# Optimization experiments

Hardware: AMD Instinct MI355X
Metric: run time of the kernel (lower is better)

The kernel has to match this reference:

```python
import jax, jax.numpy as jnp
import numpy as np

N = 2048
D = 512
E = 65536
THR = 0.0          # config['edge_threshold']
CLUSTER_RANGE = 2
NEG_SLOPE = 0.01   # F.leaky_relu default


def segment_softmax(x, seg, num_segments):
    # torch_geometric.utils.softmax over segments (here: source nodes)
    m = jax.ops.segment_max(x, seg, num_segments)
    e = jnp.exp(x - m[seg])
    s = jax.ops.segment_sum(e, seg, num_segments)
    return e / (s[seg] + 1e-16)


def setup_inputs() -> dict:
    key = jax.random.key(0)
    k1, k2, k3 = jax.random.split(key, 3)
    embedding = jax.random.normal(k1, (N, D), dtype=jnp.float32)
    edge_index = jax.random.randint(k2, (2, E), 0, N)
    src, dst = edge_index[0], edge_index[1]
    edge_matrix = jnp.zeros((N, N), jnp.float32).at[src, dst].set(1.0)
    edge_matrix_weight = edge_matrix  # unit edge weights
    W_score = (jax.random.normal(k3, (2 * D, 1), dtype=jnp.float32) / np.sqrt(2.0 * D)).astype(jnp.float32)
    b_score = jnp.zeros((1,), jnp.float32)
    return {"embedding": embedding, "edge_index": edge_index,
            "edge_matrix": edge_matrix, "edge_matrix_weight": edge_matrix_weight,
            "W_score": W_score, "b_score": b_score}


def reference(embedding, edge_index, edge_matrix, edge_matrix_weight, W_score, b_score):
    n = embedding.shape[0]
    dt = embedding.dtype
    diag = jnp.eye(n, dtype=bool)

    # connectivity fitness: Z @ Z.T with L2-normalized rows
    Z = embedding / jnp.maximum(jnp.linalg.norm(embedding, axis=-1, keepdims=True), 1e-12)
    connectivity_M = Z @ Z.T                                   # [N,N]

    # structural fitness: edge-score -> leaky_relu -> segment softmax -> dense scatter
    src, dst = edge_index[0], edge_index[1]
    x_pair = jnp.concatenate([embedding[src], embedding[dst]], axis=-1) @ W_score + b_score  # [E,1]
    x_score = jax.nn.leaky_relu(x_pair[:, 0], NEG_SLOPE)
    x_score = segment_softmax(x_score, src, n)
    structure_M = jnp.zeros((n, n), dt).at[src, dst].add(x_score)
    fitness = connectivity_M + structure_M                     # fitness_mode == 'both_j'

    # Generate_clusters (cluster_range = 2)
    mat = jnp.where(diag, 0.0, edge_matrix)
    mat = jnp.where(fitness < THR, 0.0, mat)
    A1 = mat
    A2 = (jnp.where(diag, 0.0, A1 @ A1) > 0.5).astype(dt)
    A2 = jnp.maximum(A2 - A1, 0.0)
    cluster_matrix = ((A1 + A2) > 0).astype(dt)

    # Cluster_assignment: mean fitness per cluster matrix, nan -> 0
    scores = jnp.zeros((n,), dt)
    for A in (A1, A2):
        deg = A.sum(-1)
        scores = scores + jnp.where(deg > 0, (fitness * A).sum(-1) / jnp.where(deg > 0, deg, 1.0), 0.0)
    cluster_scores = scores / CLUSTER_RANGE

    # Select_clusters (overlap=True, pick_all=True): local extrema over A1 neighborhood
    local_extrema = (cluster_scores[:, None] - A1 * cluster_scores[None, :]) > 0
    is_cluster = local_extrema.all(axis=-1)                    # boolean cluster-center mask

    # Generate_assignment_matrix (mask-based instead of column slicing; removed
    # 'reduced' columns are kept as zero columns so shapes stay static)
    S = cluster_matrix
    S_f = cluster_matrix * fitness
    reduced = (S * is_cluster.astype(dt)[None, :]).sum(-1) > 0   # member of a selected cluster
    isolated = S.sum(0) == 0
    reduced = reduced | isolated
    keeping = (~is_cluster) & (~reduced)

    S = jnp.where(keeping[None, :], 0.0, S)
    S_f = jnp.where(keeping[None, :], 0.0, S_f)
    S = jnp.where(diag, 1.0, S)
    S_f = jnp.where(diag, 1.0, S_f)
    col_keep = (~reduced).astype(dt)[None, :]
    S = S * col_keep
    S_f = S_f * col_keep

    # pooling_mode == 'mean': pooled embedding = S_w.T @ X
    pooled = S_f.T @ embedding                                  # [N, D], zero rows = removed nodes
    return pooled
```

## Files before the change

### kernel.cpp

```cpp
#include <hip/hip_runtime.h>
#include <cstdint>
#include <cstddef>

typedef unsigned long long u64;
typedef unsigned int u32;
typedef _Float16 half8 __attribute__((ext_vector_type(8)));
typedef float f32x4 __attribute__((ext_vector_type(4)));

#define NN 2048
#define DD 512
#define EE 65536
#define NW 32

__device__ __forceinline__ u32 fmap(float x) {
    u32 u = __float_as_uint(x);
    return (u & 0x80000000u) ? ~u : (u | 0x80000000u);
}
__device__ __forceinline__ float funmap(u32 u) {
    return (u & 0x80000000u) ? __uint_as_float(u ^ 0x80000000u) : __uint_as_float(~u);
}

__global__ __launch_bounds__(256) void k_node(const float* __restrict__ emb,
                                              const float* __restrict__ Wsc,
                                              float* inv_norm, float* av, float* cv,
                                              _Float16* __restrict__ zh,
                                              _Float16* __restrict__ zl,
                                              u32* mmax, float* ssum,
                                              u64* centerBits, u64* colAny, u64* EBw) {
    int n = blockIdx.x;
    int t = threadIdx.x;
    if (n < 256) EBw[n * 256 + t] = 0ull;
    else if (n < 264) { int idx = (n - 256) * 256 + t; mmax[idx] = 0u; ssum[idx] = 0.0f; }
    else if (n == 264 && t < NW) { centerBits[t] = 0ull; colAny[t] = 0ull; }

    const float* row = emb + (size_t)n * DD;
    float ss = 0.f, aa = 0.f, cc = 0.f;
    for (int d = t; d < DD; d += 256) {
        float v = row[d];
        ss += v * v;
        aa += v * Wsc[d];
        cc += v * Wsc[DD + d];
    }
    for (int off = 32; off; off >>= 1) {
        ss += __shfl_down(ss, off);
        aa += __shfl_down(aa, off);
        cc += __shfl_down(cc, off);
    }
    __shared__ float red[3][4];
    __shared__ float s_inv;
    int wid = t >> 6, lane = t & 63;
    if (lane == 0) { red[0][wid] = ss; red[1][wid] = aa; red[2][wid] = cc; }
    __syncthreads();
    if (t == 0) {
        float s = 0.f, a = 0.f, c = 0.f;
        for (int w = 0; w < 4; w++) { s += red[0][w]; a += red[1][w]; c += red[2][w]; }
        float iv = 1.0f / fmaxf(sqrtf(s), 1e-12f);
        inv_norm[n] = iv;
        s_inv = iv;
        av[n] = a;
        cv[n] = c;
    }
    __syncthreads();
    float iv = s_inv;
    for (int d = t; d < DD; d += 256) {
        float z = row[d] * iv;
        _Float16 h = (_Float16)z;
        _Float16 l = (_Float16)(z - (float)h);
        zh[(size_t)n * DD + d] = h;
        zl[(size_t)n * DD + d] = l;
    }
}

__device__ __forceinline__ float edge_score(const int* ei, const float* av, const float* cv,
                                            float b0, int e, int* src, int* dst) {
    int s = ei[e], d = ei[EE + e];
    *src = s; *dst = d;
    float x = av[s] + cv[d] + b0;
    return x > 0.f ? x : 0.01f * x;
}

__global__ __launch_bounds__(256) void k_edgeA(const int* __restrict__ ei,
                                               const float* __restrict__ av,
                                               const float* __restrict__ cv,
                                               const float* __restrict__ bsc,
                                               u32* mmax, u64* EBw) {
    int e = blockIdx.x * 256 + threadIdx.x;
    if (e >= EE) return;
    int s, d;
    float x = edge_score(ei, av, cv, bsc[0], e, &s, &d);
    atomicMax(&mmax[s], fmap(x));
    atomicOr(&EBw[(size_t)s * NW + (d >> 6)], 1ull << (d & 63));
}

__global__ __launch_bounds__(256) void k_edge_sum(const int* __restrict__ ei,
                                                  const float* __restrict__ av,
                                                  const float* __restrict__ cv,
                                                  const float* __restrict__ bsc,
                                                  const u32* __restrict__ mmax, float* ssum) {
    int e = blockIdx.x * 256 + threadIdx.x;
    if (e >= EE) return;
    int s, d;
    float x = edge_score(ei, av, cv, bsc[0], e, &s, &d);
    float w = expf(x - funmap(mmax[s]));
    atomicAdd(&ssum[s], w);
}

__global__ __launch_bounds__(256) void k_edge_scatter(const int* __restrict__ ei,
                                                      const float* __restrict__ av,
                                                      const float* __restrict__ cv,
                                                      const float* __restrict__ bsc,
                                                      const u32* __restrict__ mmax,
                                                      const float* __restrict__ ssum,
                                                      float* fit) {
    int e = blockIdx.x * 256 + threadIdx.x;
    if (e >= EE) return;
    int s, d;
    float x = edge_score(ei, av, cv, bsc[0], e, &s, &d);
    float w = expf(x - funmap(mmax[s])) / (ssum[s] + 1e-16f);
    atomicAdd(&fit[(size_t)s * NN + d], w);
}

#define BK 64
__global__ __launch_bounds__(512) void k_fitness(const _Float16* __restrict__ zh,
                                                 const _Float16* __restrict__ zl,
                                                 float* __restrict__ fit) {
    __shared__ _Float16 Ah[128 * BK];
    __shared__ _Float16 Al[128 * BK];
    __shared__ _Float16 Bh[128 * BK];
    __shared__ _Float16 Bl[128 * BK];
    int tid = threadIdx.x;
    int wid = tid >> 6, lane = tid & 63;
    int wr = wid >> 2, wc = wid & 3;
    int I = blockIdx.y * 128, J = blockIdx.x * 128;
    int lr = lane & 15;
    int q = lane >> 4;
    f32x4 acc[4][2] = {};

    int rl0 = tid >> 3, sl0 = tid & 7;
    int rl1 = (512 + tid) >> 3, sl1 = tid & 7;
    int ks0 = ((sl0 ^ (rl0 & 7)) << 3);
    int ks1 = ((sl1 ^ (rl1 & 7)) << 3);
    size_t gA0 = (size_t)(I + rl0) * DD + ks0, gB0 = (size_t)(J + rl0) * DD + ks0;
    size_t gA1 = (size_t)(I + rl1) * DD + ks1, gB1 = (size_t)(J + rl1) * DD + ks1;
    int lo0 = rl0 * BK + sl0 * 8, lo1 = rl1 * BK + sl1 * 8;

    {
        half8 a0 = *reinterpret_cast<const half8*>(&zh[gA0]);
        half8 a1 = *reinterpret_cast<const half8*>(&zh[gA1]);
        half8 l0 = *reinterpret_cast<const half8*>(&zl[gA0]);
        half8 l1 = *reinterpret_cast<const half8*>(&zl[gA1]);
        half8 b0 = *reinterpret_cast<const half8*>(&zh[gB0]);
        half8 b1 = *reinterpret_cast<const half8*>(&zh[gB1]);
        half8 m0 = *reinterpret_cast<const half8*>(&zl[gB0]);
        half8 m1 = *reinterpret_cast<const half8*>(&zl[gB1]);
        *reinterpret_cast<half8*>(&Ah[lo0]) = a0;
        *reinterpret_cast<half8*>(&Ah[lo1]) = a1;
        *reinterpret_cast<half8*>(&Al[lo0]) = l0;
        *reinterpret_cast<half8*>(&Al[lo1]) = l1;
        *reinterpret_cast<half8*>(&Bh[lo0]) = b0;
        *reinterpret_cast<half8*>(&Bh[lo1]) = b1;
        *reinterpret_cast<half8*>(&Bl[lo0]) = m0;
        *reinterpret_cast<half8*>(&Bl[lo1]) = m1;
    }
    __syncthreads();

    for (int k0 = 0; k0 < DD; k0 += BK) {
        half8 nA0, nA1, nAl0, nAl1, nB0, nB1, nBl0, nBl1;
        bool hasNext = (k0 + BK) < DD;
        if (hasNext) {
            int kn = k0 + BK;
            nA0  = *reinterpret_cast<const half8*>(&zh[gA0 + kn]);
            nA1  = *reinterpret_cast<const half8*>(&zh[gA1 + kn]);
            nAl0 = *reinterpret_cast<const half8*>(&zl[gA0 + kn]);
            nAl1 = *reinterpret_cast<const half8*>(&zl[gA1 + kn]);
            nB0  = *reinterpret_cast<const half8*>(&zh[gB0 + kn]);
            nB1  = *reinterpret_cast<const half8*>(&zh[gB1 + kn]);
            nBl0 = *reinterpret_cast<const half8*>(&zl[gB0 + kn]);
            nBl1 = *reinterpret_cast<const half8*>(&zl[gB1 + kn]);
        }
#pragma unroll
        for (int kk = 0; kk < 2; kk++) {
            half8 a_h[4], a_l[4], b_h[2], b_l[2];
#pragma unroll
            for (int f = 0; f < 4; f++) {
                int ra = wr * 64 + f * 16 + lr;
                int ca = (kk * 4 + q) ^ (ra & 7);
                int oa = ra * BK + ca * 8;
                a_h[f] = *reinterpret_cast<const half8*>(&Ah[oa]);
                a_l[f] = *reinterpret_cast<const half8*>(&Al[oa]);
            }
#pragma unroll
            for (int v = 0; v < 2; v++) {
                int rb = wc * 32 + v * 16 + lr;
                int cb = (kk * 4 + q) ^ (rb & 7);
                int ob = rb * BK + cb * 8;
                b_h[v] = *reinterpret_cast<const half8*>(&Bh[ob]);
                b_l[v] = *reinterpret_cast<const half8*>(&Bl[ob]);
            }
#pragma unroll
            for (int u = 0; u < 4; u++)
#pragma unroll
                for (int v = 0; v < 2; v++) {
                    acc[u][v] = __builtin_amdgcn_mfma_f32_16x16x32_f16(a_h[u], b_h[v], acc[u][v], 0, 0, 0);
                    acc[u][v] = __builtin_amdgcn_mfma_f32_16x16x32_f16(a_h[u], b_l[v], acc[u][v], 0, 0, 0);
                    acc[u][v] = __builtin_amdgcn_mfma_f32_16x16x32_f16(a_l[u], b_h[v], acc[u][v], 0, 0, 0);
                }
        }
        if (hasNext) {
            __syncthreads();
            *reinterpret_cast<half8*>(&Ah[lo0]) = nA0;
            *reinterpret_cast<half8*>(&Ah[lo1]) = nA1;
            *reinterpret_cast<half8*>(&Al[lo0]) = nAl0;
            *reinterpret_cast<half8*>(&Al[lo1]) = nAl1;
            *reinterpret_cast<half8*>(&Bh[lo0]) = nB0;
            *reinterpret_cast<half8*>(&Bh[lo1]) = nB1;
            *reinterpret_cast<half8*>(&Bl[lo0]) = nBl0;
            *reinterpret_cast<half8*>(&Bl[lo1]) = nBl1;
            __syncthreads();
        }
    }
#pragma unroll
    for (int u = 0; u < 4; u++) {
        int r = I + wr * 64 + u * 16 + q * 4;
#pragma unroll
        for (int v = 0; v < 2; v++) {
            int c = J + wc * 32 + v * 16 + lr;
#pragma unroll
            for (int i2 = 0; i2 < 4; i2++)
                fit[(size_t)(r + i2) * NN + c] = acc[u][v][i2];
        }
    }
}

__global__ void k_bits(const u64* __restrict__ EBw, const float* __restrict__ fit,
                       u64* __restrict__ A1w) {
    int i = blockIdx.x;
    int t = threadIdx.x;
    int lane = t & 63, wv = t >> 6;
    for (int q = 0; q < 8; q++) {
        int j = q * 256 + t;
        u64 eb = EBw[(size_t)i * NW + (j >> 6)];
        float f = fit[(size_t)i * NN + j];
        bool pred = ((eb >> (j & 63)) & 1) && (j != i) && (f >= 0.f);
        u64 word = __ballot(pred);
        if (lane == 0) A1w[i * NW + q * 4 + wv] = word;
    }
}

__global__ __launch_bounds__(256) void k_paths2s(const u64* __restrict__ A1w,
                                                 const float* __restrict__ fit,
                                                 u64* __restrict__ A2w, u64* __restrict__ CLw,
                                                 float* cs) {
    int i = blockIdx.x;
    __shared__ u64 rowA[NW];
    __shared__ u64 rowA2[NW];
    __shared__ u64 part[8][NW];
    int t = threadIdx.x;
    if (t < NW) rowA[t] = A1w[i * NW + t];
    __syncthreads();
    int g = t >> 5, w = t & 31;
    u64 acc = 0;
    for (int ww = 0; ww < 4; ww++) {
        u64 bits = rowA[g * 4 + ww];
        int kbase = (g * 4 + ww) * 64;
        while (bits) {
            int k = __ffsll((unsigned long long)bits) - 1;
            bits &= bits - 1;
            acc |= A1w[(size_t)(kbase + k) * NW + w];
        }
    }
    part[g][w] = acc;
    __syncthreads();
    if (g == 0) {
        u64 p2 = part[0][w];
#pragma unroll
        for (int gg = 1; gg < 8; gg++) p2 |= part[gg][w];
        if ((i >> 6) == w) p2 &= ~(1ull << (i & 63));
        u64 a1 = rowA[w];
        u64 a2 = p2 & ~a1;
        u64 cl = a1 | a2;
        A2w[i * NW + w] = a2;
        CLw[i * NW + w] = cl;
        rowA2[w] = a2;
    }
    __syncthreads();
    float s1 = 0.f, s2 = 0.f;
    int d1 = 0, d2 = 0;
    for (int q = 0; q < 8; q++) {
        int j = q * 256 + t;
        float f = fit[(size_t)i * NN + j];
        int ww = j >> 6, b = j & 63;
        u64 a1 = rowA[ww], a2 = rowA2[ww];
        if ((a1 >> b) & 1) { s1 += f; d1++; }
        if ((a2 >> b) & 1) { s2 += f; d2++; }
    }
    for (int off = 32; off; off >>= 1) {
        s1 += __shfl_down(s1, off);
        s2 += __shfl_down(s2, off);
        d1 += __shfl_down(d1, off);
        d2 += __shfl_down(d2, off);
    }
    __shared__ float rs1[4], rs2[4];
    __shared__ int rd1[4], rd2[4];
    int wid = t >> 6, lane = t & 63;
    if (lane == 0) { rs1[wid] = s1; rs2[wid] = s2; rd1[wid] = d1; rd2[wid] = d2; }
    __syncthreads();
    if (t == 0) {
        float S1 = 0.f, S2 = 0.f; int D1 = 0, D2 = 0;
        for (int w2 = 0; w2 < 4; w2++) { S1 += rs1[w2]; S2 += rs2[w2]; D1 += rd1[w2]; D2 += rd2[w2]; }
        float v1 = D1 > 0 ? S1 / (float)D1 : 0.f;
        float v2 = D2 > 0 ? S2 / (float)D2 : 0.f;
        cs[i] = 0.5f * (v1 + v2);
    }
}

__global__ __launch_bounds__(256) void k_extcol(const u64* __restrict__ A1w,
                                                const u64* __restrict__ CLw,
                                                const float* __restrict__ cs,
                                                unsigned char* is_c, u64* centerBits,
                                                u64* colAny) {
    int i = blockIdx.x, t = threadIdx.x;
    __shared__ u64 part[8][NW];
    if (i < 64) {
        int sub = t >> 5, w = t & 31;
        u64 acc = 0;
#pragma unroll
        for (int k = 0; k < 4; k++) {
            int r = i * 32 + sub + k * 8;
            acc |= CLw[(size_t)r * NW + w];
        }
        part[sub][w] = acc;
    }
    float ci = cs[i];
    int ok = 1;
    for (int q = 0; q < 8; q++) {
        int j = q * 256 + t;
        u64 a1 = A1w[i * NW + (j >> 6)];
        float other = ((a1 >> (j & 63)) & 1) ? cs[j] : 0.0f;
        ok &= ((ci - other) > 0.0f) ? 1 : 0;
    }
    int all = __syncthreads_and(ok);
    if (t == 0) {
        is_c[i] = (unsigned char)(all ? 1 : 0);
        if (all) atomicOr(&centerBits[i >> 6], 1ull << (i & 63));
    }
    if (i < 64 && t < NW) {
        u64 v = part[0][t];
#pragma unroll
        for (int s = 1; s < 8; s++) v |= part[s][t];
        atomicOr(&colAny[t], v);
    }
}

__global__ __launch_bounds__(256) void k_pooled(const float* __restrict__ fit,
                                                const float* __restrict__ emb,
                                                const u64* __restrict__ CLw,
                                                const u64* __restrict__ centerBits,
                                                const u64* __restrict__ colAny,
                                                const unsigned char* __restrict__ is_c,
                                                float* __restrict__ out) {
    int j = blockIdx.x;
    int t = threadIdx.x;
    bool red = ((colAny[j >> 6] >> (j & 63)) & 1ull) == 0ull;
    for (int w = 0; w < NW; w++) red |= (CLw[(size_t)j * NW + w] & centerBits[w]) != 0ull;
    const float2* embj = reinterpret_cast<const float2*>(emb + (size_t)j * DD);
    float2* outj = reinterpret_cast<float2*>(out + (size_t)j * DD);
    bool active = is_c[j] && !red;
    if (!active) {
        float dg = red ? 0.0f : 1.0f;
        float2 v = embj[t];
        float2 o; o.x = v.x * dg; o.y = v.y * dg;
        outj[t] = o;
        return;
    }
    __shared__ int lidx[NN];
    __shared__ float lwt[NN];
    __shared__ int wcnt[4];
    int wid = t >> 6, lane = t & 63;
    int wsh = j >> 6;
    u64 bmask = 1ull << (j & 63);
    int total = 0;
    for (int qq = 0; qq < 8; qq++) {
        int i = qq * 256 + t;
        u64 cw = CLw[(size_t)i * NW + wsh];
        bool p = (cw & bmask) != 0ull;
        float f = 0.f;
        if (p) f = fit[(size_t)i * NN + j];
        u64 mask = __ballot(p);
        if (lane == 0) wcnt[wid] = __popcll(mask);
        __syncthreads();
        int off = total;
        for (int w = 0; w < wid; w++) off += wcnt[w];
        int tq = wcnt[0] + wcnt[1] + wcnt[2] + wcnt[3];
        if (p) {
            int pos = off + __popcll(mask & ((1ull << lane) - 1ull));
            lidx[pos] = i;
            lwt[pos] = f;
        }
        total += tq;
        __syncthreads();
    }
    float2 acc = {0.f, 0.f};
    int k = 0;
    for (; k + 16 <= total; k += 16) {
        int idxr[16];
        float wtr[16];
#pragma unroll
        for (int u = 0; u < 16; u++) { idxr[u] = lidx[k + u]; wtr[u] = lwt[k + u]; }
        float2 e[16];
#pragma unroll
        for (int u = 0; u < 16; u++)
            e[u] = reinterpret_cast<const float2*>(emb + (size_t)idxr[u] * DD)[t];
#pragma unroll
        for (int u = 0; u < 16; u++) {
            acc.x += wtr[u] * e[u].x;
            acc.y += wtr[u] * e[u].y;
        }
    }
    for (; k < total; k++) {
        int i = lidx[k];
        float w = lwt[k];
        float2 e = reinterpret_cast<const float2*>(emb + (size_t)i * DD)[t];
        acc.x += w * e.x;
        acc.y += w * e.y;
    }
    float2 v = embj[t];
    acc.x += v.x;
    acc.y += v.y;
    outj[t] = acc;
}

extern "C" void kernel_launch(void* const* d_in, const int* in_sizes, int n_in,
                              void* d_out, int out_size, void* d_ws, size_t ws_size,
                              hipStream_t stream) {
    const float* emb = (const float*)d_in[0];
    const int*   ei  = (const int*)d_in[1];
    const float* Wsc = (const float*)d_in[4];
    const float* bsc = (const float*)d_in[5];
    float* out = (float*)d_out;

    char* ws = (char*)d_ws;
    size_t off = 0;
    auto alloc = [&](size_t bytes) -> char* {
        char* p = ws + off;
        off = (off + bytes + 255) & ~(size_t)255;
        return p;
    };
    float* fit  = (float*)alloc((size_t)NN * NN * 4);
    char*  zblk = alloc((size_t)2 * NN * DD * 2);
    _Float16* zh = (_Float16*)zblk;
    _Float16* zl = (_Float16*)(zblk + (size_t)NN * DD * 2);
    u64* A1w = (u64*)zblk;
    u64* A2w = (u64*)(zblk + (size_t)NN * NW * 8);
    u64* CLw = (u64*)(zblk + (size_t)2 * NN * NW * 8);
    u64*   EBw        = (u64*)alloc((size_t)NN * NW * 8);
    u64*   centerBits = (u64*)alloc(NW * 8);
    u64*   colAny     = (u64*)alloc(NW * 8);
    float* inv_norm   = (float*)alloc(NN * 4);
    float* av         = (float*)alloc(NN * 4);
    float* cv         = (float*)alloc(NN * 4);
    float* ssum       = (float*)alloc(NN * 4);
    float* cs         = (float*)alloc(NN * 4);
    u32*   mmax       = (u32*)alloc(NN * 4);
    unsigned char* is_c = (unsigned char*)alloc(NN);

    k_node<<<dim3(NN), dim3(256), 0, stream>>>(emb, Wsc, inv_norm, av, cv, zh, zl,
                                               mmax, ssum, centerBits, colAny, EBw);
    k_edgeA<<<dim3(EE / 256), dim3(256), 0, stream>>>(ei, av, cv, bsc, mmax, EBw);
    k_edge_sum<<<dim3(EE / 256), dim3(256), 0, stream>>>(ei, av, cv, bsc, mmax, ssum);
    k_fitness<<<dim3(NN / 128, NN / 128), dim3(512), 0, stream>>>(zh, zl, fit);
    k_edge_scatter<<<dim3(EE / 256), dim3(256), 0, stream>>>(ei, av, cv, bsc, mmax, ssum, fit);
    k_bits<<<dim3(NN), dim3(256), 0, stream>>>(EBw, fit, A1w);
    k_paths2s<<<dim3(NN), dim3(256), 0, stream>>>(A1w, fit, A2w, CLw, cs);
    k_extcol<<<dim3(NN), dim3(256), 0, stream>>>(A1w, CLw, cs, is_c, centerBits, colAny);
    k_pooled<<<dim3(NN), dim3(256), 0, stream>>>(fit, emb, CLw, centerBits, colAny, is_c, out);
}
```

Measured before the change: 157.3 us.

## Drop softmax max pass and compute only upper-triangle Gram tiles

The segment softmax no longer subtracts a per-source max, so the atomicMax kernel pass and the separate sum kernel merge into one edge pass that accumulates exp(x) directly. The Gram matrix kernel now launches only the 136 upper-triangle 128x128 tiles and writes each off-diagonal tile's transpose through shared memory, exploiting symmetry of Z Z^T to halve MFMA work. Removing the max shift risks overflow for large scores, though the scores here are small. The transposed store adds shared-memory traffic and a second global write per tile.

```diff
diff --git a/kernel.cpp b/kernel.cpp
--- a/kernel.cpp
+++ b/kernel.cpp
@@ -11,26 +11,18 @@
 #define DD 512
 #define EE 65536
 #define NW 32
-
-__device__ __forceinline__ u32 fmap(float x) {
-    u32 u = __float_as_uint(x);
-    return (u & 0x80000000u) ? ~u : (u | 0x80000000u);
-}
-__device__ __forceinline__ float funmap(u32 u) {
-    return (u & 0x80000000u) ? __uint_as_float(u ^ 0x80000000u) : __uint_as_float(~u);
-}
 
 __global__ __launch_bounds__(256) void k_node(const float* __restrict__ emb,
                                               const float* __restrict__ Wsc,
                                               float* inv_norm, float* av, float* cv,
                                               _Float16* __restrict__ zh,
                                               _Float16* __restrict__ zl,
-                                              u32* mmax, float* ssum,
+                                              float* ssum,
                                               u64* centerBits, u64* colAny, u64* EBw) {
     int n = blockIdx.x;
     int t = threadIdx.x;
     if (n < 256) EBw[n * 256 + t] = 0ull;
-    else if (n < 264) { int idx = (n - 256) * 256 + t; mmax[idx] = 0u; ssum[idx] = 0.0f; }
+    else if (n < 264) { int idx = (n - 256) * 256 + t; ssum[idx] = 0.0f; }
     else if (n == 264 && t < NW) { centerBits[t] = 0ull; colAny[t] = 0ull; }
 
     const float* row = emb + (size_t)n * DD;
@@ -83,40 +75,26 @@
                                                const float* __restrict__ av,
                                                const float* __restrict__ cv,
                                                const float* __restrict__ bsc,
-                                               u32* mmax, u64* EBw) {
+                                               float* ssum, u64* EBw) {
     int e = blockIdx.x * 256 + threadIdx.x;
     if (e >= EE) return;
     int s, d;
     float x = edge_score(ei, av, cv, bsc[0], e, &s, &d);
-    atomicMax(&mmax[s], fmap(x));
+    atomicAdd(&ssum[s], expf(x));
     atomicOr(&EBw[(size_t)s * NW + (d >> 6)], 1ull << (d & 63));
-}
-
-__global__ __launch_bounds__(256) void k_edge_sum(const int* __restrict__ ei,
-                                                  const float* __restrict__ av,
-                                                  const float* __restrict__ cv,
-                                                  const float* __restrict__ bsc,
-                                                  const u32* __restrict__ mmax, float* ssum) {
-    int e = blockIdx.x * 256 + threadIdx.x;
-    if (e >= EE) return;
-    int s, d;
-    float x = edge_score(ei, av, cv, bsc[0], e, &s, &d);
-    float w = expf(x - funmap(mmax[s]));
-    atomicAdd(&ssum[s], w);
 }
 
 __global__ __launch_bounds__(256) void k_edge_scatter(const int* __restrict__ ei,
                                                       const float* __restrict__ av,
                                                       const float* __restrict__ cv,
                                                       const float* __restrict__ bsc,
-                                                      const u32* __restrict__ mmax,
                                                       const float* __restrict__ ssum,
                                                       float* fit) {
     int e = blockIdx.x * 256 + threadIdx.x;
     if (e >= EE) return;
     int s, d;
     float x = edge_score(ei, av, cv, bsc[0], e, &s, &d);
-    float w = expf(x - funmap(mmax[s])) / (ssum[s] + 1e-16f);
+    float w = expf(x) / (ssum[s] + 1e-16f);
     atomicAdd(&fit[(size_t)s * NN + d], w);
 }
 
@@ -124,14 +102,18 @@
 __global__ __launch_bounds__(512) void k_fitness(const _Float16* __restrict__ zh,
                                                  const _Float16* __restrict__ zl,
                                                  float* __restrict__ fit) {
-    __shared__ _Float16 Ah[128 * BK];
-    __shared__ _Float16 Al[128 * BK];
-    __shared__ _Float16 Bh[128 * BK];
-    __shared__ _Float16 Bl[128 * BK];
+    __shared__ _Float16 SM[4 * 128 * BK];
+    _Float16* Ah = SM;
+    _Float16* Al = SM + 128 * BK;
+    _Float16* Bh = SM + 2 * 128 * BK;
+    _Float16* Bl = SM + 3 * 128 * BK;
     int tid = threadIdx.x;
     int wid = tid >> 6, lane = tid & 63;
     int wr = wid >> 2, wc = wid & 3;
-    int I = blockIdx.y * 128, J = blockIdx.x * 128;
+    int p = blockIdx.x, bi = 0;
+    while (p >= 16 - bi) { p -= 16 - bi; bi++; }
+    int bj = bi + p;
+    int I = bi * 128, J = bj * 128;
     int lr = lane & 15;
     int q = lane >> 4;
     f32x4 acc[4][2] = {};
@@ -228,6 +210,25 @@
 #pragma unroll
             for (int i2 = 0; i2 < 4; i2++)
                 fit[(size_t)(r + i2) * NN + c] = acc[u][v][i2];
+        }
+    }
+    if (bi != bj) {
+        __syncthreads();
+        float* Tw = reinterpret_cast<float*>(SM) + wid * 1040;
+#pragma unroll
+        for (int v = 0; v < 2; v++) {
+#pragma unroll
+            for (int u = 0; u < 4; u++)
+#pragma unroll
+                for (int i2 = 0; i2 < 4; i2++)
+                    Tw[lr * 65 + u * 16 + q * 4 + i2] = acc[u][v][i2];
+            int cbase = J + wc * 32 + v * 16;
+            int rbase = I + wr * 64;
+#pragma unroll
+            for (int rr = 0; rr < 16; rr++) {
+                float val = Tw[rr * 65 + lane];
+                fit[(size_t)(cbase + rr) * NN + rbase + lane] = val;
+            }
         }
     }
 }
@@ -461,15 +462,13 @@
     float* cv         = (float*)alloc(NN * 4);
     float* ssum       = (float*)alloc(NN * 4);
     float* cs         = (float*)alloc(NN * 4);
-    u32*   mmax       = (u32*)alloc(NN * 4);
     unsigned char* is_c = (unsigned char*)alloc(NN);
 
     k_node<<<dim3(NN), dim3(256), 0, stream>>>(emb, Wsc, inv_norm, av, cv, zh, zl,
-                                               mmax, ssum, centerBits, colAny, EBw);
-    k_edgeA<<<dim3(EE / 256), dim3(256), 0, stream>>>(ei, av, cv, bsc, mmax, EBw);
-    k_edge_sum<<<dim3(EE / 256), dim3(256), 0, stream>>>(ei, av, cv, bsc, mmax, ssum);
-    k_fitness<<<dim3(NN / 128, NN / 128), dim3(512), 0, stream>>>(zh, zl, fit);
-    k_edge_scatter<<<dim3(EE / 256), dim3(256), 0, stream>>>(ei, av, cv, bsc, mmax, ssum, fit);
+                                               ssum, centerBits, colAny, EBw);
+    k_edgeA<<<dim3(EE / 256), dim3(256), 0, stream>>>(ei, av, cv, bsc, ssum, EBw);
+    k_fitness<<<dim3(136), dim3(512), 0, stream>>>(zh, zl, fit);
+    k_edge_scatter<<<dim3(EE / 256), dim3(256), 0, stream>>>(ei, av, cv, bsc, ssum, fit);
     k_bits<<<dim3(NN), dim3(256), 0, stream>>>(EBw, fit, A1w);
     k_paths2s<<<dim3(NN), dim3(256), 0, stream>>>(A1w, fit, A2w, CLw, cs);
     k_extcol<<<dim3(NN), dim3(256), 0, stream>>>(A1w, CLw, cs, is_c, centerBits, colAny);
```

Result: faster. 148.9 us (-5.3%).
